# Performance work log

Hardware: AMD Instinct MI355X
Metric: run time of the kernel (lower is better)

The kernel has to match this reference:

```python
import jax, jax.numpy as jnp
import numpy as np

B, T, N, D, INTER, KS = 8, 12, 325, 64, 16, 3
BN_EPS = 1e-5
LN_EPS = 1e-5


def _stx(x):
    # [B,T,N,D] -> edge-pad time, unfold window 3 -> [B,T,3N,D] (window-major like torch reshape)
    xp = jnp.concatenate([x[:, :1], x, x[:, -1:]], axis=1)          # [B,T+2,N,D]
    w = jnp.stack([xp[:, i:i + T] for i in range(3)], axis=2)        # [B,T,3,N,D]
    return w.reshape(x.shape[0], T, 3 * N, x.shape[-1])


def _conv1x1(y, W, b):
    # y: [B,C,T,N], W: [O,C], b: [O]
    return jnp.einsum('bctn,oc->botn', y, W) + b[None, :, None, None]


def _bn_eval(y, g, b):
    # BatchNorm2d eval with running mean 0 / var 1
    return y * (g / jnp.sqrt(1.0 + BN_EPS))[None, :, None, None] + b[None, :, None, None]


def setup_inputs() -> dict:
    key = jax.random.key(0)
    ks = jax.random.split(key, 32)
    inp = {}
    inp['x'] = jax.random.normal(ks[0], (B, T, N, D), jnp.float32)
    inp['gso'] = jax.random.normal(ks[1], (B, N, N), jnp.float32) * 0.05
    inp['geo_mask'] = jax.random.bernoulli(ks[2], 0.5, (N, N))
    s = 1.0 / np.sqrt(D)
    inp['Wq'] = jax.random.normal(ks[3], (D, D), jnp.float32) * s
    inp['Wk'] = jax.random.normal(ks[4], (D, D), jnp.float32) * s
    inp['Wv'] = jax.random.normal(ks[5], (D, D), jnp.float32) * s
    inp['cheb_w'] = jax.random.normal(ks[6], (KS, D, D), jnp.float32) * s
    inp['p_t12'] = jax.random.normal(ks[7], (N,), jnp.float32)
    inp['p_t21'] = jax.random.normal(ks[8], (N,), jnp.float32)
    inp['p_t23'] = jax.random.normal(ks[9], (N,), jnp.float32)
    inp['p_t32'] = jax.random.normal(ks[10], (N,), jnp.float32)
    inp['ln_g'] = jnp.ones((D,), jnp.float32)
    inp['ln_b'] = jnp.zeros((D,), jnp.float32)
    si = 1.0 / np.sqrt(INTER)
    for pfx, kk in (('l', 11), ('g', 17)):
        inp[pfx + '_w1'] = jax.random.normal(ks[kk], (INTER, D), jnp.float32) * s
        inp[pfx + '_b1'] = jax.random.normal(ks[kk + 1], (INTER,), jnp.float32) * s
        inp[pfx + '_g1'] = jnp.ones((INTER,), jnp.float32)
        inp[pfx + '_be1'] = jnp.zeros((INTER,), jnp.float32)
        inp[pfx + '_w2'] = jax.random.normal(ks[kk + 2], (D, INTER), jnp.float32) * si
        inp[pfx + '_b2'] = jax.random.normal(ks[kk + 3], (D,), jnp.float32) * si
        inp[pfx + '_g2'] = jnp.ones((D,), jnp.float32)
        inp[pfx + '_be2'] = jnp.zeros((D,), jnp.float32)
    return inp


def _forward(x, gso, geo_mask, Wq, Wk, Wv, cheb_w, p_t12, p_t21, p_t23, p_t32,
             ln_g, ln_b,
             l_w1, l_b1, l_g1, l_be1, l_w2, l_b2, l_g2, l_be2,
             g_w1, g_b1, g_g1, g_be1, g_w2, g_b2, g_g2, g_be2):
    M = 3 * N
    stX = _stx(x)                                                    # [B,T,M,D]

    # ---- DSTFormer: masked spatiotemporal attention (no scaling, per source) ----
    q = jnp.einsum('btmd,od->btmo', stX, Wq)
    k = jnp.einsum('btmd,od->btmo', stX, Wk)
    v = jnp.einsum('btmd,od->btmo', stX, Wv)
    attn = jnp.einsum('btmo,btno->btmn', q, k)                       # [B,T,M,M]
    eye = jnp.eye(N, dtype=bool)
    uneye = ~eye
    tru = jnp.ones((N, N), dtype=bool)
    big_mask = jnp.block([[geo_mask, uneye, tru],
                          [uneye, geo_mask, uneye],
                          [tru, uneye, geo_mask]])                   # [M,M]
    attn = jnp.where(big_mask, -jnp.inf, attn)
    p = jax.nn.softmax(attn, axis=-1)
    sem = jnp.einsum('btmn,btno->btmo', p, v)                        # [B,T,M,D]
    # faithful to torch: transpose(2,3) then reshape(B,T,M,-1) (mixes layout)
    y = jnp.swapaxes(sem, 2, 3).reshape(B, T, M, D)
    attn_out = y.reshape(B, T, 3, N, D)[:, :, 1]                     # [B,T,N,D]

    # ---- DSTGCN: Chebyshev conv on assembled [B,3N,3N] shift operator ----
    Z = jnp.zeros((B, N, N), x.dtype)
    dg = lambda vv: jnp.broadcast_to(jnp.diag(vv), (B, N, N))
    row0 = jnp.concatenate([gso, dg(p_t21), Z], axis=2)
    row1 = jnp.concatenate([dg(p_t12), gso, dg(p_t32)], axis=2)
    row2 = jnp.concatenate([Z, dg(p_t23), gso], axis=2)
    L = jnp.concatenate([row0, row1, row2], axis=1)                  # [B,M,M]
    xs = [stX, jnp.einsum('bhi,btij->bthj', L, stX)]
    for kk in range(2, KS):
        xs.append(jnp.einsum('bhi,btij->bthj', 2.0 * L, xs[kk - 1]) - xs[kk - 2])
    xk = jnp.stack(xs, axis=2)                                       # [B,T,KS,M,D]
    h = jnp.einsum('btkhi,kij->bthj', xk, cheb_w)                    # [B,T,M,D]
    h = jnp.transpose(h, (0, 3, 1, 2)).reshape(B, D, T, 3, N)[:, :, :, 1, :]  # [B,D,T,N]
    h = jnp.transpose(h, (0, 2, 3, 1))                               # [B,T,N,D]
    mu = h.mean(-1, keepdims=True)
    var = ((h - mu) ** 2).mean(-1, keepdims=True)
    gcn_out = (h - mu) / jnp.sqrt(var + LN_EPS) * ln_g + ln_b

    # ---- AFF fusion on channel-first maps ----
    xc = jnp.transpose(attn_out, (0, 3, 1, 2))                       # [B,D,T,N]
    rc = jnp.transpose(gcn_out, (0, 3, 1, 2))
    xa = xc + rc
    zl = jax.nn.relu(_bn_eval(_conv1x1(xa, l_w1, l_b1), l_g1, l_be1))
    xl = _bn_eval(_conv1x1(zl, l_w2, l_b2), l_g2, l_be2)
    m = xa.mean((2, 3), keepdims=True)
    zg = jax.nn.relu(_bn_eval(_conv1x1(m, g_w1, g_b1), g_g1, g_be1))
    xg = _bn_eval(_conv1x1(zg, g_w2, g_b2), g_g2, g_be2)
    wei = jax.nn.sigmoid(xl + xg)
    out = 2.0 * xc * wei + 2.0 * rc * (1.0 - wei)
    return jnp.transpose(out, (0, 2, 3, 1))                          # [B,T,N,D]


def reference(x, gso, geo_mask, Wq, Wk, Wv, cheb_w, p_t12, p_t21, p_t23, p_t32,
              ln_g, ln_b,
              l_w1, l_b1, l_g1, l_be1, l_w2, l_b2, l_g2, l_be2,
              g_w1, g_b1, g_g1, g_be1, g_w2, g_b2, g_g2, g_be2):
    return _forward(x, gso, geo_mask, Wq, Wk, Wv, cheb_w, p_t12, p_t21, p_t23, p_t32,
                    ln_g, ln_b,
                    l_w1, l_b1, l_g1, l_be1, l_w2, l_b2, l_g2, l_be2,
                    g_w1, g_b1, g_g1, g_be1, g_w2, g_b2, g_g2, g_be2)
```

## Files before the change

kernel.cpp:

```cpp
#include <hip/hip_runtime.h>
#include <math.h>

constexpr int TT = 12;
constexpr int NN = 325;
constexpr int MM = 975;
constexpr int DD = 64;
constexpr long SZ = 96L * MM * DD;
constexpr int GSTR = 352;
constexpr int MBSTR = 48;
constexpr float BN_EPS_ = 1e-5f;
constexpr float LN_EPS_ = 1e-5f;

constexpr long WS_MASKB = 0;
constexpr long WS_GSOB  = WS_MASKB + 4096;
constexpr long WS_STXB  = WS_GSOB + 457600;
constexpr long WS_QB    = WS_STXB + SZ / 2;
constexpr long WS_KB    = WS_QB + SZ / 2;
constexpr long WS_VB    = WS_KB + SZ / 2;
constexpr long WS_SEM   = WS_VB + SZ / 2;
constexpr long WS_T2B   = WS_SEM + SZ;
constexpr long WS_MBD   = WS_T2B + 998400;

typedef _Float16 half8 __attribute__((ext_vector_type(8)));
typedef __attribute__((ext_vector_type(4))) float f32x4;

static __device__ inline unsigned short f2h(float f) {
  _Float16 h = (_Float16)f;
  return __builtin_bit_cast(unsigned short, h);
}
static __device__ inline float h2f(unsigned short s) {
  return (float)__builtin_bit_cast(_Float16, s);
}

__global__ __launch_bounds__(256) void k_maskprep(const unsigned char* __restrict__ raw,
                                                  unsigned char* __restrict__ outm) {
  bool is_u8 = false;
  for (int i = 0; i < 256; ++i) {
    if (raw[4 * i + 1]) { is_u8 = true; break; }
  }
  int idx = blockIdx.x * 256 + threadIdx.x;
  if (idx >= NN * MBSTR) return;
  int n = idx / MBSTR, jb = idx - n * MBSTR;
  unsigned char v = 0;
  for (int k = 0; k < 8; ++k) {
    int col = jb * 8 + k;
    bool m = true;
    if (col < NN) {
      int f = n * NN + col;
      m = is_u8 ? (raw[f] != 0) : (((const int*)raw)[f] != 0);
    }
    v |= (unsigned char)(m ? 1 : 0) << k;
  }
  outm[idx] = v;
}

__global__ __launch_bounds__(256) void k_gsoprep(const float* __restrict__ gso,
                                                 unsigned short* __restrict__ gsoB) {
  int idx = blockIdx.x * 256 + threadIdx.x;
  int b = idx / (NN * GSTR);
  int rem = idx - b * (NN * GSTR);
  int r = rem / GSTR, j = rem - r * GSTR;
  gsoB[idx] = (j < NN) ? f2h(gso[(long)b * NN * NN + r * NN + j]) : (unsigned short)0;
}

__global__ __launch_bounds__(256) void k_stx(const float* __restrict__ x,
                                             unsigned short* __restrict__ stXb) {
  int idx = blockIdx.x * 256 + threadIdx.x;
  int d = idx & 63;
  int m = (idx >> 6) % MM;
  int bt = idx / (MM * DD);
  int b = bt / TT, t = bt - b * TT;
  int w = m / NN, n = m - w * NN;
  int st = t + w - 1;
  st = st < 0 ? 0 : (st > TT - 1 ? TT - 1 : st);
  stXb[idx] = f2h(x[(((b * TT + st) * NN + n) << 6) + d]);
}

__global__ __launch_bounds__(256) void k_qkv_mfma(const unsigned short* __restrict__ stXb,
                                                  const float* __restrict__ Wq,
                                                  const float* __restrict__ Wk,
                                                  const float* __restrict__ Wv,
                                                  unsigned short* __restrict__ qb,
                                                  unsigned short* __restrict__ kb,
                                                  unsigned short* __restrict__ vb) {
  __shared__ alignas(16) unsigned short sX[128 * 72];
  __shared__ alignas(16) unsigned short sW[64 * 72];
  const float* W = blockIdx.y == 0 ? Wq : (blockIdx.y == 1 ? Wk : Wv);
  unsigned short* outb = blockIdx.y == 0 ? qb : (blockIdx.y == 1 ? kb : vb);
  int tid = threadIdx.x;
  long r0 = (long)blockIdx.x * 128;
  for (int u = 0; u < 4; ++u) {
    int idx = tid + 256 * u;
    int row = idx >> 3, c8 = idx & 7;
    long rg = r0 + row; if (rg > 93599) rg = 93599;
    *(uint4*)&sX[row * 72 + c8 * 8] = *(const uint4*)&stXb[rg * 64 + c8 * 8];
  }
  for (int u = 0; u < 16; ++u) {
    int f = tid + 256 * u;
    int o = f >> 6, d = f & 63;
    sW[o * 72 + d] = f2h(W[f]);
  }
  __syncthreads();
  int lane = tid & 63;
  int wv = __builtin_amdgcn_readfirstlane(tid >> 6);
  int lr = lane & 15, lg = lane >> 4;
  f32x4 zero4 = {0.f, 0.f, 0.f, 0.f};
  f32x4 acc[2][4];
#pragma unroll
  for (int rt = 0; rt < 2; ++rt)
#pragma unroll
    for (int c = 0; c < 4; ++c) acc[rt][c] = zero4;
#pragma unroll
  for (int kk = 0; kk < 2; ++kk) {
    half8 a0 = *(const half8*)&sX[(32 * wv + lr) * 72 + kk * 32 + lg * 8];
    half8 a1 = *(const half8*)&sX[(32 * wv + 16 + lr) * 72 + kk * 32 + lg * 8];
#pragma unroll
    for (int c = 0; c < 4; ++c) {
      half8 b = *(const half8*)&sW[(16 * c + lr) * 72 + kk * 32 + lg * 8];
      acc[0][c] = __builtin_amdgcn_mfma_f32_16x16x32_f16(a0, b, acc[0][c], 0, 0, 0);
      acc[1][c] = __builtin_amdgcn_mfma_f32_16x16x32_f16(a1, b, acc[1][c], 0, 0, 0);
    }
  }
  __syncthreads();
#pragma unroll
  for (int rt = 0; rt < 2; ++rt)
#pragma unroll
    for (int c = 0; c < 4; ++c)
#pragma unroll
      for (int e = 0; e < 4; ++e) {
        int row = 32 * wv + 16 * rt + lg * 4 + e;
        int col = 16 * c + lr;
        sX[row * 64 + col] = f2h(acc[rt][c][e]);
      }
  __syncthreads();
  for (int u = 0; u < 4; ++u) {
    int idx = tid + 256 * u;
    int row = idx >> 3, c8 = idx & 7;
    long rg = r0 + row;
    if (rg < 93600)
      *(uint4*)&outb[rg * 64 + c8 * 8] = *(const uint4*)&sX[row * 64 + c8 * 8];
  }
}

__global__ __launch_bounds__(256) void k_attn(const unsigned short* __restrict__ qb,
                                              const unsigned short* __restrict__ kb,
                                              const unsigned short* __restrict__ vb,
                                              const unsigned char* __restrict__ maskb,
                                              float* __restrict__ sem) {
  __shared__ alignas(16) unsigned short Kl[336 * 72];
  __shared__ alignas(16) unsigned short Ql[64 * 72];
  __shared__ unsigned char Mb[64 * MBSTR];
  int btw = blockIdx.x;
  int bt = btw / 3, w = btw - bt * 3;
  int rt = blockIdx.y;
  long base = ((long)bt * MM + (long)w * NN) * 64;
  int tid = threadIdx.x;
  for (int u = 0; u < 11; ++u) {
    int idx = tid + 256 * u;
    if (idx < 2688) {
      int r = idx >> 3, c8 = idx & 7;
      int rr = r < NN ? r : NN - 1;
      *(uint4*)&Kl[r * 72 + c8 * 8] = *(const uint4*)&kb[base + (long)rr * 64 + c8 * 8];
    }
  }
  for (int u = 0; u < 2; ++u) {
    int idx = tid + 256 * u;
    int r = idx >> 3, c8 = idx & 7;
    int rg = rt * 64 + r; if (rg > NN - 1) rg = NN - 1;
    *(uint4*)&Ql[r * 72 + c8 * 8] = *(const uint4*)&qb[base + (long)rg * 64 + c8 * 8];
  }
  if (tid < 192) {
    int r = tid / 3, c16 = tid - (tid / 3) * 3;
    int rg = rt * 64 + r; if (rg > NN - 1) rg = NN - 1;
    *(uint4*)&Mb[r * MBSTR + c16 * 16] = *(const uint4*)&maskb[(long)rg * MBSTR + c16 * 16];
  }
  __syncthreads();
  int lane = tid & 63;
  int wv = __builtin_amdgcn_readfirstlane(tid >> 6);
  int lr = lane & 15, lg = lane >> 4;
  f32x4 zero4 = {0.f, 0.f, 0.f, 0.f};
  f32x4 acc[22];
#pragma unroll
  for (int ct = 0; ct < 22; ++ct) acc[ct] = zero4;
  f32x4 dA = zero4, dB = zero4;
  int nl_f = rt * 64 + 16 * wv + lr; if (nl_f > NN - 1) nl_f = NN - 1;
  long pAaddr = ((long)bt * MM + ((w == 1) ? nl_f : NN + nl_f)) * 64;
  long pBaddr = ((long)bt * MM + 2 * NN + nl_f) * 64;
#pragma unroll
  for (int kk = 0; kk < 2; ++kk) {
    half8 a = *(const half8*)&Ql[(16 * wv + lr) * 72 + kk * 32 + lg * 8];
#pragma unroll
    for (int ct = 0; ct < 21; ++ct) {
      half8 b = *(const half8*)&Kl[(16 * ct + lr) * 72 + kk * 32 + lg * 8];
      acc[ct] = __builtin_amdgcn_mfma_f32_16x16x32_f16(a, b, acc[ct], 0, 0, 0);
    }
    half8 bA = *(const half8*)&kb[pAaddr + kk * 32 + lg * 8];
    dA = __builtin_amdgcn_mfma_f32_16x16x32_f16(a, bA, dA, 0, 0, 0);
    if (w == 1) {
      half8 bB = *(const half8*)&kb[pBaddr + kk * 32 + lg * 8];
      dB = __builtin_amdgcn_mfma_f32_16x16x32_f16(a, bB, dB, 0, 0, 0);
    }
  }
  float da_[4], db_[4];
#pragma unroll
  for (int e = 0; e < 4; ++e) {
    int src = lg * 20 + e;
    da_[e] = __shfl(dA[e], src);
    db_[e] = (w == 1) ? __shfl(dB[e], src) : -INFINITY;
  }
  float mx[4] = {-INFINITY, -INFINITY, -INFINITY, -INFINITY};
#pragma unroll
  for (int ct = 0; ct < 22; ++ct) {
    int col = 16 * ct + lr;
#pragma unroll
    for (int e = 0; e < 4; ++e) {
      int rl = 16 * wv + lg * 4 + e;
      bool masked = (col >= NN) ||
                    ((Mb[rl * MBSTR + (col >> 3)] >> (col & 7)) & 1);
      float s = masked ? -INFINITY : acc[ct][e];
      acc[ct][e] = s;
      mx[e] = fmaxf(mx[e], s);
    }
  }
#pragma unroll
  for (int e = 0; e < 4; ++e)
    for (int m = 1; m < 16; m <<= 1) mx[e] = fmaxf(mx[e], __shfl_xor(mx[e], m));
  float gm[4], ea[4], eb[4], sum[4], inv[4];
#pragma unroll
  for (int e = 0; e < 4; ++e) {
    gm[e] = fmaxf(mx[e], da_[e]);
    if (w == 1) gm[e] = fmaxf(gm[e], db_[e]);
    sum[e] = 0.f;
  }
#pragma unroll
  for (int ct = 0; ct < 22; ++ct)
#pragma unroll
    for (int e = 0; e < 4; ++e) {
      float s = acc[ct][e];
      float p = (s > -1e37f) ? __expf(s - gm[e]) : 0.f;
      acc[ct][e] = p;
      sum[e] += p;
    }
#pragma unroll
  for (int e = 0; e < 4; ++e) {
    for (int m = 1; m < 16; m <<= 1) sum[e] += __shfl_xor(sum[e], m);
    ea[e] = __expf(da_[e] - gm[e]);
    eb[e] = (w == 1) ? __expf(db_[e] - gm[e]) : 0.f;
    sum[e] += ea[e] + eb[e];
    inv[e] = 1.f / sum[e];
  }
  __syncthreads();
  unsigned short* Bt = Kl;
  for (int u = 0; u < 22; ++u) {
    int idx = tid + 256 * u;
    if (idx < 5632) {
      int k = idx >> 4, c4 = idx & 15;
      ushort4 vvv;
      if (k < NN) vvv = *(const ushort4*)&vb[base + (long)k * 64 + c4 * 4];
      else { vvv.x = 0; vvv.y = 0; vvv.z = 0; vvv.w = 0; }
      Bt[(4 * c4 + 0) * 352 + k] = vvv.x;
      Bt[(4 * c4 + 1) * 352 + k] = vvv.y;
      Bt[(4 * c4 + 2) * 352 + k] = vvv.z;
      Bt[(4 * c4 + 3) * 352 + k] = vvv.w;
    }
  }
  __syncthreads();
  unsigned short* Ptr = (unsigned short*)Ql + wv * 640;
  f32x4 oacc[4];
#pragma unroll
  for (int c = 0; c < 4; ++c) oacc[c] = zero4;
  for (int ck = 0; ck < 11; ++ck) {
#pragma unroll
    for (int t = 0; t < 2; ++t) {
      int ct = 2 * ck + t;
#pragma unroll
      for (int e = 0; e < 4; ++e)
        Ptr[(lg * 4 + e) * 40 + t * 16 + lr] = f2h(acc[ct][e] * inv[e]);
    }
    half8 a = *(const half8*)&Ptr[lr * 40 + lg * 8];
#pragma unroll
    for (int c = 0; c < 4; ++c) {
      half8 b = *(const half8*)&Bt[(16 * c + lr) * 352 + ck * 32 + lg * 8];
      oacc[c] = __builtin_amdgcn_mfma_f32_16x16x32_f16(a, b, oacc[c], 0, 0, 0);
    }
  }
#pragma unroll
  for (int c = 0; c < 4; ++c)
#pragma unroll
    for (int e = 0; e < 4; ++e) {
      int n = rt * 64 + 16 * wv + lg * 4 + e;
      int col = 16 * c + lr;
      if (n < NN) {
        float val = oacc[c][e];
        int partA = (w == 1) ? n : NN + n;
        val += ea[e] * inv[e] * h2f(vb[((long)bt * MM + partA) * 64 + col]);
        if (w == 1)
          val += eb[e] * inv[e] * h2f(vb[((long)bt * MM + 2 * NN + n) * 64 + col]);
        sem[((long)bt * MM + (long)w * NN + n) * 64 + col] = val;
      }
    }
}

__global__ __launch_bounds__(256) void k_xs1_mfma(const unsigned short* __restrict__ gsoB,
                                                  const unsigned short* __restrict__ stXb,
                                                  const float* __restrict__ pt12,
                                                  const float* __restrict__ pt21,
                                                  const float* __restrict__ pt23,
                                                  const float* __restrict__ pt32,
                                                  unsigned short* __restrict__ xs1b) {
  __shared__ alignas(16) unsigned short Al[128 * 40];
  __shared__ alignas(16) unsigned short Bt[64 * 40];
  int btw = blockIdx.x;
  int bt = btw / 3, w = btw - bt * 3;
  int b = bt / TT;
  int rt_blk = blockIdx.y;
  const unsigned short* A = gsoB + (long)b * NN * GSTR;
  long vbase = (long)bt * MM + (long)w * NN;
  int tid = threadIdx.x;
  int lane = tid & 63;
  int wv = __builtin_amdgcn_readfirstlane(tid >> 6);
  int lr = lane & 15, lg = lane >> 4;
  f32x4 zero4 = {0.f, 0.f, 0.f, 0.f};
  f32x4 acc[2][4];
#pragma unroll
  for (int rt = 0; rt < 2; ++rt)
#pragma unroll
    for (int c = 0; c < 4; ++c) acc[rt][c] = zero4;
  for (int kb_ = 0; kb_ < 352; kb_ += 32) {
    __syncthreads();
    for (int u = 0; u < 2; ++u) {
      int idx = tid + 256 * u;
      int row = idx >> 2, c8 = idx & 3;
      int rr = rt_blk * 128 + row; if (rr > NN - 1) rr = NN - 1;
      *(uint4*)&Al[row * 40 + c8 * 8] = *(const uint4*)&A[(long)rr * GSTR + kb_ + c8 * 8];
    }
    for (int u = 0; u < 2; ++u) {
      int idx = tid + 256 * u;
      int k = idx >> 4, c4 = idx & 15;
      int kg = kb_ + k;
      ushort4 vv;
      if (kg < NN) vv = *(const ushort4*)&stXb[(vbase + kg) * 64 + c4 * 4];
      else { vv.x = 0; vv.y = 0; vv.z = 0; vv.w = 0; }
      Bt[(4 * c4 + 0) * 40 + k] = vv.x;
      Bt[(4 * c4 + 1) * 40 + k] = vv.y;
      Bt[(4 * c4 + 2) * 40 + k] = vv.z;
      Bt[(4 * c4 + 3) * 40 + k] = vv.w;
    }
    __syncthreads();
    half8 a0 = *(const half8*)&Al[(32 * wv + lr) * 40 + lg * 8];
    half8 a1 = *(const half8*)&Al[(32 * wv + 16 + lr) * 40 + lg * 8];
#pragma unroll
    for (int c = 0; c < 4; ++c) {
      half8 b_ = *(const half8*)&Bt[(16 * c + lr) * 40 + lg * 8];
      acc[0][c] = __builtin_amdgcn_mfma_f32_16x16x32_f16(a0, b_, acc[0][c], 0, 0, 0);
      acc[1][c] = __builtin_amdgcn_mfma_f32_16x16x32_f16(a1, b_, acc[1][c], 0, 0, 0);
    }
  }
  long btM = (long)bt * MM;
#pragma unroll
  for (int rt = 0; rt < 2; ++rt)
#pragma unroll
    for (int c = 0; c < 4; ++c)
#pragma unroll
      for (int e = 0; e < 4; ++e) {
        int n = rt_blk * 128 + 32 * wv + 16 * rt + lg * 4 + e;
        int col = 16 * c + lr;
        if (n < NN) {
          float val = acc[rt][c][e];
          if (w == 0) {
            val += pt21[n] * h2f(stXb[(btM + NN + n) * 64 + col]);
          } else if (w == 1) {
            val += pt12[n] * h2f(stXb[(btM + n) * 64 + col])
                 + pt32[n] * h2f(stXb[(btM + 2 * NN + n) * 64 + col]);
          } else {
            val += pt23[n] * h2f(stXb[(btM + NN + n) * 64 + col]);
          }
          xs1b[(btM + (long)w * NN + n) * 64 + col] = f2h(val);
        }
      }
}

__global__ __launch_bounds__(256) void k_t2_mfma(const unsigned short* __restrict__ gsoB,
                                                 const unsigned short* __restrict__ xs1b,
                                                 const unsigned short* __restrict__ stXb,
                                                 const float* __restrict__ pt12,
                                                 const float* __restrict__ pt32,
                                                 unsigned short* __restrict__ t2b) {
  __shared__ alignas(16) unsigned short Al[128 * 40];
  __shared__ alignas(16) unsigned short Bt[64 * 40];
  int bt = blockIdx.x;
  int b = bt / TT;
  int rt_blk = blockIdx.y;
  const unsigned short* A = gsoB + (long)b * NN * GSTR;
  long vbase = (long)bt * MM + NN;
  int tid = threadIdx.x;
  int lane = tid & 63;
  int wv = __builtin_amdgcn_readfirstlane(tid >> 6);
  int lr = lane & 15, lg = lane >> 4;
  f32x4 zero4 = {0.f, 0.f, 0.f, 0.f};
  f32x4 acc[2][4];
#pragma unroll
  for (int rt = 0; rt < 2; ++rt)
#pragma unroll
    for (int c = 0; c < 4; ++c) acc[rt][c] = zero4;
  for (int kb_ = 0; kb_ < 352; kb_ += 32) {
    __syncthreads();
    for (int u = 0; u < 2; ++u) {
      int idx = tid + 256 * u;
      int row = idx >> 2, c8 = idx & 3;
      int rr = rt_blk * 128 + row; if (rr > NN - 1) rr = NN - 1;
      *(uint4*)&Al[row * 40 + c8 * 8] = *(const uint4*)&A[(long)rr * GSTR + kb_ + c8 * 8];
    }
    for (int u = 0; u < 2; ++u) {
      int idx = tid + 256 * u;
      int k = idx >> 4, c4 = idx & 15;
      int kg = kb_ + k;
      ushort4 vv;
      if (kg < NN) vv = *(const ushort4*)&xs1b[(vbase + kg) * 64 + c4 * 4];
      else { vv.x = 0; vv.y = 0; vv.z = 0; vv.w = 0; }
      Bt[(4 * c4 + 0) * 40 + k] = vv.x;
      Bt[(4 * c4 + 1) * 40 + k] = vv.y;
      Bt[(4 * c4 + 2) * 40 + k] = vv.z;
      Bt[(4 * c4 + 3) * 40 + k] = vv.w;
    }
    __syncthreads();
    half8 a0 = *(const half8*)&Al[(32 * wv + lr) * 40 + lg * 8];
    half8 a1 = *(const half8*)&Al[(32 * wv + 16 + lr) * 40 + lg * 8];
#pragma unroll
    for (int c = 0; c < 4; ++c) {
      half8 b_ = *(const half8*)&Bt[(16 * c + lr) * 40 + lg * 8];
      acc[0][c] = __builtin_amdgcn_mfma_f32_16x16x32_f16(a0, b_, acc[0][c], 0, 0, 0);
      acc[1][c] = __builtin_amdgcn_mfma_f32_16x16x32_f16(a1, b_, acc[1][c], 0, 0, 0);
    }
  }
  long btM = (long)bt * MM;
#pragma unroll
  for (int rt = 0; rt < 2; ++rt)
#pragma unroll
    for (int c = 0; c < 4; ++c)
#pragma unroll
      for (int e = 0; e < 4; ++e) {
        int n = rt_blk * 128 + 32 * wv + 16 * rt + lg * 4 + e;
        int col = 16 * c + lr;
        if (n < NN) {
          float val = 2.f * (pt12[n] * h2f(xs1b[(btM + n) * 64 + col])
                             + acc[rt][c][e]
                             + pt32[n] * h2f(xs1b[(btM + 2 * NN + n) * 64 + col]))
                      - h2f(stXb[(btM + NN + n) * 64 + col]);
          t2b[((long)bt * NN + n) * 64 + col] = f2h(val);
        }
      }
}

__global__ __launch_bounds__(256) void k_cheb_mfma(const unsigned short* __restrict__ stXb,
                                                   const unsigned short* __restrict__ xs1b,
                                                   const unsigned short* __restrict__ t2b,
                                                   const float* __restrict__ cw,
                                                   const float* __restrict__ lng,
                                                   const float* __restrict__ lnb,
                                                   float* __restrict__ gcn) {
  __shared__ alignas(16) unsigned short Bt[64 * 200];
  __shared__ alignas(16) unsigned short Al[128 * 40];
  int tid = threadIdx.x;
  for (int u = 0; u < 48; ++u) {
    int f = tid + 256 * u;
    int K = f >> 6, j = f & 63;
    Bt[j * 200 + K] = f2h(cw[f]);
  }
  int lane = tid & 63;
  int wv = __builtin_amdgcn_readfirstlane(tid >> 6);
  int lr = lane & 15, lg = lane >> 4;
  long grow0 = (long)blockIdx.x * 128;
  f32x4 zero4 = {0.f, 0.f, 0.f, 0.f};
  f32x4 acc[2][4];
#pragma unroll
  for (int rt = 0; rt < 2; ++rt)
#pragma unroll
    for (int c = 0; c < 4; ++c) acc[rt][c] = zero4;
  for (int ch = 0; ch < 6; ++ch) {
    const unsigned short* src = ch < 2 ? stXb : (ch < 4 ? xs1b : t2b);
    int koff = (ch & 1) * 32;
    __syncthreads();
    for (int u = 0; u < 2; ++u) {
      int idx = tid + 256 * u;
      int row = idx >> 2, c8 = idx & 3;
      long gr = grow0 + row; if (gr > 31199) gr = 31199;
      int bt = (int)(gr / NN), n = (int)(gr - (long)bt * NN);
      long sbase = (ch < 4) ? ((long)bt * MM + NN + n) * 64 : gr * 64;
      *(uint4*)&Al[row * 40 + c8 * 8] = *(const uint4*)&src[sbase + koff + c8 * 8];
    }
    __syncthreads();
    half8 a0 = *(const half8*)&Al[(32 * wv + lr) * 40 + lg * 8];
    half8 a1 = *(const half8*)&Al[(32 * wv + 16 + lr) * 40 + lg * 8];
#pragma unroll
    for (int c = 0; c < 4; ++c) {
      half8 b = *(const half8*)&Bt[(16 * c + lr) * 200 + ch * 32 + lg * 8];
      acc[0][c] = __builtin_amdgcn_mfma_f32_16x16x32_f16(a0, b, acc[0][c], 0, 0, 0);
      acc[1][c] = __builtin_amdgcn_mfma_f32_16x16x32_f16(a1, b, acc[1][c], 0, 0, 0);
    }
  }
  float lngv[4], lnbv[4];
#pragma unroll
  for (int c = 0; c < 4; ++c) { lngv[c] = lng[16 * c + lr]; lnbv[c] = lnb[16 * c + lr]; }
#pragma unroll
  for (int rt = 0; rt < 2; ++rt)
#pragma unroll
    for (int e = 0; e < 4; ++e) {
      float s = acc[rt][0][e] + acc[rt][1][e] + acc[rt][2][e] + acc[rt][3][e];
      for (int m = 1; m < 16; m <<= 1) s += __shfl_xor(s, m);
      float mu = s * (1.f / 64.f);
      float q = 0.f;
#pragma unroll
      for (int c = 0; c < 4; ++c) { float d = acc[rt][c][e] - mu; q += d * d; }
      for (int m = 1; m < 16; m <<= 1) q += __shfl_xor(q, m);
      float rstd = rsqrtf(q * (1.f / 64.f) + LN_EPS_);
      long gr = grow0 + 32 * wv + 16 * rt + lg * 4 + e;
      if (gr < 31200) {
#pragma unroll
        for (int c = 0; c < 4; ++c)
          gcn[gr * 64 + 16 * c + lr] = (acc[rt][c][e] - mu) * rstd * lngv[c] + lnbv[c];
      }
    }
}

__global__ __launch_bounds__(256) void k_mean(const float* __restrict__ sem,
                                              const float* __restrict__ gcn,
                                              float* __restrict__ mbd) {
  __shared__ float red[4][64];
  int bt = blockIdx.x;
  int b = bt / TT;
  int d = threadIdx.x & 63, g = threadIdx.x >> 6;
  float s = 0.f;
  for (int n = g; n < NN; n += 4) {
    int f = (NN + n) * 64 + d;
    int mm = f % MM, ii = f / MM;
    float a = sem[((long)bt * MM + mm) * 64 + ii];
    float r = gcn[((long)bt * NN + n) * 64 + d];
    s += a + r;
  }
  red[g][d] = s;
  __syncthreads();
  if (threadIdx.x < 64) {
    float v = red[0][d] + red[1][d] + red[2][d] + red[3][d];
    atomicAdd(&mbd[b * 64 + d], v);
  }
}

__global__ __launch_bounds__(64) void k_glob(const float* __restrict__ mbd,
                                             const float* __restrict__ w1,
                                             const float* __restrict__ b1,
                                             const float* __restrict__ g1,
                                             const float* __restrict__ be1,
                                             const float* __restrict__ w2,
                                             const float* __restrict__ b2,
                                             const float* __restrict__ g2,
                                             const float* __restrict__ be2,
                                             float* __restrict__ xg) {
  __shared__ float ml[64];
  __shared__ float zg[16];
  int b = blockIdx.x, d = threadIdx.x;
  ml[d] = mbd[b * 64 + d] * (1.f / 3900.f);
  __syncthreads();
  float rb = rsqrtf(1.f + BN_EPS_);
  if (d < 16) {
    float a = b1[d];
    for (int i = 0; i < 64; ++i) a += w1[d * 64 + i] * ml[i];
    a = a * (g1[d] * rb) + be1[d];
    zg[d] = a > 0.f ? a : 0.f;
  }
  __syncthreads();
  float a = b2[d];
  for (int i = 0; i < 16; ++i) a += w2[d * 16 + i] * zg[i];
  xg[b * 64 + d] = a * (g2[d] * rb) + be2[d];
}

__global__ __launch_bounds__(256) void k_final(const float* __restrict__ sem,
                                               const float* __restrict__ gcn,
                                               const float* __restrict__ xg,
                                               const float* __restrict__ w1,
                                               const float* __restrict__ b1,
                                               const float* __restrict__ g1,
                                               const float* __restrict__ be1,
                                               const float* __restrict__ w2,
                                               const float* __restrict__ b2,
                                               const float* __restrict__ g2,
                                               const float* __restrict__ be2,
                                               float* __restrict__ out) {
  __shared__ float w1l[16][65];
  __shared__ float w2l[64][17];
  __shared__ float xal[4][64];
  __shared__ float zll[4][16];
  int tid = threadIdx.x;
  for (int u = 0; u < 4; ++u) {
    int f = tid + 256 * u;
    w1l[f >> 6][f & 63] = w1[f];
    w2l[f >> 4][f & 15] = w2[f];
  }
  int lane = tid & 63, wv = tid >> 6;
  long row = (long)blockIdx.x * 4 + wv;
  int bt = (int)(row / NN);
  int n = (int)(row - (long)bt * NN);
  int b = bt / TT;
  int f = (NN + n) * 64 + lane;
  int mm = f % MM, ii = f / MM;
  float a = sem[((long)bt * MM + mm) * 64 + ii];
  float r = gcn[row * DD + lane];
  float xa = a + r;
  xal[wv][lane] = xa;
  __syncthreads();
  float rb = rsqrtf(1.f + BN_EPS_);
  if (lane < 16) {
    float acc = b1[lane];
#pragma unroll 8
    for (int i = 0; i < 64; ++i) acc += w1l[lane][i] * xal[wv][i];
    acc = acc * (g1[lane] * rb) + be1[lane];
    zll[wv][lane] = acc > 0.f ? acc : 0.f;
  }
  __syncthreads();
  float acc = b2[lane];
#pragma unroll
  for (int i = 0; i < 16; ++i) acc += w2l[lane][i] * zll[wv][i];
  float xl = acc * (g2[lane] * rb) + be2[lane];
  float wei = 1.f / (1.f + __expf(-(xl + xg[b * 64 + lane])));
  out[row * DD + lane] = 2.f * a * wei + 2.f * r * (1.f - wei);
}

extern "C" void kernel_launch(void* const* d_in, const int* in_sizes, int n_in,
                              void* d_out, int out_size, void* d_ws, size_t ws_size,
                              hipStream_t stream) {
  const float* x    = (const float*)d_in[0];
  const float* gso  = (const float*)d_in[1];
  const unsigned char* mask_raw = (const unsigned char*)d_in[2];
  const float* Wq   = (const float*)d_in[3];
  const float* Wk   = (const float*)d_in[4];
  const float* Wv   = (const float*)d_in[5];
  const float* chw  = (const float*)d_in[6];
  const float* pt12 = (const float*)d_in[7];
  const float* pt21 = (const float*)d_in[8];
  const float* pt23 = (const float*)d_in[9];
  const float* pt32 = (const float*)d_in[10];
  const float* lng  = (const float*)d_in[11];
  const float* lnb  = (const float*)d_in[12];
  const float* l_w1 = (const float*)d_in[13];
  const float* l_b1 = (const float*)d_in[14];
  const float* l_g1 = (const float*)d_in[15];
  const float* l_be1= (const float*)d_in[16];
  const float* l_w2 = (const float*)d_in[17];
  const float* l_b2 = (const float*)d_in[18];
  const float* l_g2 = (const float*)d_in[19];
  const float* l_be2= (const float*)d_in[20];
  const float* g_w1 = (const float*)d_in[21];
  const float* g_b1 = (const float*)d_in[22];
  const float* g_g1 = (const float*)d_in[23];
  const float* g_be1= (const float*)d_in[24];
  const float* g_w2 = (const float*)d_in[25];
  const float* g_b2 = (const float*)d_in[26];
  const float* g_g2 = (const float*)d_in[27];
  const float* g_be2= (const float*)d_in[28];

  float* base = (float*)d_ws;
  unsigned char* maskb = (unsigned char*)d_ws;
  unsigned short* gsoB = (unsigned short*)(base + WS_GSOB);
  unsigned short* stXb = (unsigned short*)(base + WS_STXB);
  unsigned short* qb   = (unsigned short*)(base + WS_QB);
  unsigned short* kb   = (unsigned short*)(base + WS_KB);
  unsigned short* vb   = (unsigned short*)(base + WS_VB);
  float* sem           = base + WS_SEM;
  unsigned short* t2b  = (unsigned short*)(base + WS_T2B);

  unsigned short* xs1b = vb;
  float* gcn = (float*)qb;
  float* mbd = base + WS_MBD;
  float* xg  = mbd + 512;

  k_maskprep<<<(NN * MBSTR + 255) / 256, 256, 0, stream>>>(mask_raw, maskb);
  k_gsoprep<<<3575, 256, 0, stream>>>(gso, gsoB);
  k_stx<<<23400, 256, 0, stream>>>(x, stXb);
  {
    dim3 g(732, 3);
    k_qkv_mfma<<<g, 256, 0, stream>>>(stXb, Wq, Wk, Wv, qb, kb, vb);
  }
  {
    dim3 ga(288, 6);
    k_attn<<<ga, 256, 0, stream>>>(qb, kb, vb, maskb, sem);
  }
  {
    dim3 g(288, 3);
    k_xs1_mfma<<<g, 256, 0, stream>>>(gsoB, stXb, pt12, pt21, pt23, pt32, xs1b);
  }
  {
    dim3 g(96, 3);
    k_t2_mfma<<<g, 256, 0, stream>>>(gsoB, xs1b, stXb, pt12, pt32, t2b);
  }
  k_cheb_mfma<<<244, 256, 0, stream>>>(stXb, xs1b, t2b, chw, lng, lnb, gcn);
  hipMemsetAsync(mbd, 0, 1024 * sizeof(float), stream);
  k_mean<<<96, 256, 0, stream>>>(sem, gcn, mbd);
  k_glob<<<8, 64, 0, stream>>>(mbd, g_w1, g_b1, g_g1, g_be1, g_w2, g_b2, g_g2, g_be2, xg);
  k_final<<<7800, 256, 0, stream>>>(sem, gcn, xg,
                                    l_w1, l_b1, l_g1, l_be1,
                                    l_w2, l_b2, l_g2, l_be2,
                                    (float*)d_out);
}
```

Before: 413.1 us.

## Pre-transpose V, read Q/K directly from global in attention, store fp16 output

Adds a k_vT kernel that writes V transposed into a padded workspace, so k_attn no longer transposes V in shared memory. k_attn also drops its large K/Q shared-memory staging and reads MFMA operands straight from global/L2, with launch bounds set for more resident blocks. Mask bits are now loaded as 32-bit words. The attention output becomes fp16, which halves traffic into k_mean and k_final at some precision cost. The V transposes in the xs1/t2 kernels are also rewritten as strided per-element loads.

After: 370.1 us. 10.4% less time.

```diff
diff --git a/kernel.cpp b/kernel.cpp
--- a/kernel.cpp
+++ b/kernel.cpp
@@ -8,6 +8,7 @@
 constexpr long SZ = 96L * MM * DD;
 constexpr int GSTR = 352;
 constexpr int MBSTR = 48;
+constexpr int VTS = 22528;
 constexpr float BN_EPS_ = 1e-5f;
 constexpr float LN_EPS_ = 1e-5f;
 
@@ -17,8 +18,9 @@
 constexpr long WS_QB    = WS_STXB + SZ / 2;
 constexpr long WS_KB    = WS_QB + SZ / 2;
 constexpr long WS_VB    = WS_KB + SZ / 2;
-constexpr long WS_SEM   = WS_VB + SZ / 2;
-constexpr long WS_T2B   = WS_SEM + SZ;
+constexpr long WS_VT    = WS_VB + SZ / 2;
+constexpr long WS_SEMH  = WS_VT + 3244032;
+constexpr long WS_T2B   = WS_SEMH + SZ / 2;
 constexpr long WS_MBD   = WS_T2B + 998400;
 
 typedef _Float16 half8 __attribute__((ext_vector_type(8)));
@@ -142,33 +144,49 @@
   }
 }
 
-__global__ __launch_bounds__(256) void k_attn(const unsigned short* __restrict__ qb,
-                                              const unsigned short* __restrict__ kb,
-                                              const unsigned short* __restrict__ vb,
-                                              const unsigned char* __restrict__ maskb,
-                                              float* __restrict__ sem) {
-  __shared__ alignas(16) unsigned short Kl[336 * 72];
-  __shared__ alignas(16) unsigned short Ql[64 * 72];
+__global__ __launch_bounds__(256) void k_vT(const unsigned short* __restrict__ vb,
+                                            unsigned short* __restrict__ vbT) {
+  __shared__ alignas(16) unsigned short T[128 * 72];
+  int seg = blockIdx.x;
+  int ck = blockIdx.y;
+  int tid = threadIdx.x;
+  long base = (long)seg * NN * 64;
+  int k0 = ck * 128;
+  for (int u = 0; u < 4; ++u) {
+    int idx = tid + 256 * u;
+    int row = idx >> 3, c8 = idx & 7;
+    int kg = k0 + row;
+    uint4 v;
+    if (kg < NN) v = *(const uint4*)&vb[base + (long)kg * 64 + c8 * 8];
+    else { v.x = 0; v.y = 0; v.z = 0; v.w = 0; }
+    *(uint4*)&T[row * 72 + c8 * 8] = v;
+  }
+  __syncthreads();
+  int d = tid & 63, k8 = tid >> 6;
+  for (int it = 0; it < 4; ++it) {
+    int klocal = (it * 4 + k8) * 8;
+    if (k0 + klocal < 352) {
+      unsigned short tmp[8];
+#pragma unroll
+      for (int j = 0; j < 8; ++j) tmp[j] = T[(klocal + j) * 72 + d];
+      *(uint4*)&vbT[(long)seg * VTS + (long)d * 352 + k0 + klocal] = *(const uint4*)tmp;
+    }
+  }
+}
+
+__global__ __launch_bounds__(256, 3) void k_attn(const unsigned short* __restrict__ qb,
+                                                 const unsigned short* __restrict__ kb,
+                                                 const unsigned short* __restrict__ vb,
+                                                 const unsigned short* __restrict__ vbT,
+                                                 const unsigned char* __restrict__ maskb,
+                                                 unsigned short* __restrict__ semh) {
   __shared__ unsigned char Mb[64 * MBSTR];
-  int btw = blockIdx.x;
-  int bt = btw / 3, w = btw - bt * 3;
+  __shared__ alignas(16) unsigned short Ptr4[4 * 16 * 40];
+  int seg = blockIdx.x;
+  int bt = seg / 3, w = seg - bt * 3;
   int rt = blockIdx.y;
-  long base = ((long)bt * MM + (long)w * NN) * 64;
+  long segbase = (long)seg * NN * 64;
   int tid = threadIdx.x;
-  for (int u = 0; u < 11; ++u) {
-    int idx = tid + 256 * u;
-    if (idx < 2688) {
-      int r = idx >> 3, c8 = idx & 7;
-      int rr = r < NN ? r : NN - 1;
-      *(uint4*)&Kl[r * 72 + c8 * 8] = *(const uint4*)&kb[base + (long)rr * 64 + c8 * 8];
-    }
-  }
-  for (int u = 0; u < 2; ++u) {
-    int idx = tid + 256 * u;
-    int r = idx >> 3, c8 = idx & 7;
-    int rg = rt * 64 + r; if (rg > NN - 1) rg = NN - 1;
-    *(uint4*)&Ql[r * 72 + c8 * 8] = *(const uint4*)&qb[base + (long)rg * 64 + c8 * 8];
-  }
   if (tid < 192) {
     int r = tid / 3, c16 = tid - (tid / 3) * 3;
     int rg = rt * 64 + r; if (rg > NN - 1) rg = NN - 1;
@@ -179,19 +197,22 @@
   int wv = __builtin_amdgcn_readfirstlane(tid >> 6);
   int lr = lane & 15, lg = lane >> 4;
   f32x4 zero4 = {0.f, 0.f, 0.f, 0.f};
-  f32x4 acc[22];
-#pragma unroll
-  for (int ct = 0; ct < 22; ++ct) acc[ct] = zero4;
+  f32x4 acc[21];
+#pragma unroll
+  for (int ct = 0; ct < 21; ++ct) acc[ct] = zero4;
   f32x4 dA = zero4, dB = zero4;
-  int nl_f = rt * 64 + 16 * wv + lr; if (nl_f > NN - 1) nl_f = NN - 1;
+  int arow = rt * 64 + 16 * wv + lr; if (arow > NN - 1) arow = NN - 1;
+  long abase = segbase + (long)arow * 64;
+  int nl_f = arow;
   long pAaddr = ((long)bt * MM + ((w == 1) ? nl_f : NN + nl_f)) * 64;
   long pBaddr = ((long)bt * MM + 2 * NN + nl_f) * 64;
 #pragma unroll
   for (int kk = 0; kk < 2; ++kk) {
-    half8 a = *(const half8*)&Ql[(16 * wv + lr) * 72 + kk * 32 + lg * 8];
+    half8 a = *(const half8*)&qb[abase + kk * 32 + lg * 8];
 #pragma unroll
     for (int ct = 0; ct < 21; ++ct) {
-      half8 b = *(const half8*)&Kl[(16 * ct + lr) * 72 + kk * 32 + lg * 8];
+      int brow = 16 * ct + lr; if (brow > NN - 1) brow = NN - 1;
+      half8 b = *(const half8*)&kb[segbase + (long)brow * 64 + kk * 32 + lg * 8];
       acc[ct] = __builtin_amdgcn_mfma_f32_16x16x32_f16(a, b, acc[ct], 0, 0, 0);
     }
     half8 bA = *(const half8*)&kb[pAaddr + kk * 32 + lg * 8];
@@ -209,14 +230,20 @@
     db_[e] = (w == 1) ? __shfl(dB[e], src) : -INFINITY;
   }
   float mx[4] = {-INFINITY, -INFINITY, -INFINITY, -INFINITY};
-#pragma unroll
-  for (int ct = 0; ct < 22; ++ct) {
-    int col = 16 * ct + lr;
+  unsigned mw[4];
+#pragma unroll
+  for (int ct = 0; ct < 21; ++ct) {
+    if ((ct & 1) == 0) {
+#pragma unroll
+      for (int e = 0; e < 4; ++e) {
+        int rl = 16 * wv + lg * 4 + e;
+        mw[e] = *(const unsigned*)&Mb[rl * MBSTR + (ct >> 1) * 4];
+      }
+    }
+    int sh = 16 * (ct & 1) + lr;
 #pragma unroll
     for (int e = 0; e < 4; ++e) {
-      int rl = 16 * wv + lg * 4 + e;
-      bool masked = (col >= NN) ||
-                    ((Mb[rl * MBSTR + (col >> 3)] >> (col & 7)) & 1);
+      bool masked = (mw[e] >> sh) & 1;
       float s = masked ? -INFINITY : acc[ct][e];
       acc[ct][e] = s;
       mx[e] = fmaxf(mx[e], s);
@@ -233,7 +260,7 @@
     sum[e] = 0.f;
   }
 #pragma unroll
-  for (int ct = 0; ct < 22; ++ct)
+  for (int ct = 0; ct < 21; ++ct)
 #pragma unroll
     for (int e = 0; e < 4; ++e) {
       float s = acc[ct][e];
@@ -249,38 +276,26 @@
     sum[e] += ea[e] + eb[e];
     inv[e] = 1.f / sum[e];
   }
-  __syncthreads();
-  unsigned short* Bt = Kl;
-  for (int u = 0; u < 22; ++u) {
-    int idx = tid + 256 * u;
-    if (idx < 5632) {
-      int k = idx >> 4, c4 = idx & 15;
-      ushort4 vvv;
-      if (k < NN) vvv = *(const ushort4*)&vb[base + (long)k * 64 + c4 * 4];
-      else { vvv.x = 0; vvv.y = 0; vvv.z = 0; vvv.w = 0; }
-      Bt[(4 * c4 + 0) * 352 + k] = vvv.x;
-      Bt[(4 * c4 + 1) * 352 + k] = vvv.y;
-      Bt[(4 * c4 + 2) * 352 + k] = vvv.z;
-      Bt[(4 * c4 + 3) * 352 + k] = vvv.w;
-    }
-  }
-  __syncthreads();
-  unsigned short* Ptr = (unsigned short*)Ql + wv * 640;
+  unsigned short* Ptr = Ptr4 + wv * 640;
+  long vtbase = (long)seg * VTS;
   f32x4 oacc[4];
 #pragma unroll
   for (int c = 0; c < 4; ++c) oacc[c] = zero4;
+#pragma unroll
   for (int ck = 0; ck < 11; ++ck) {
 #pragma unroll
     for (int t = 0; t < 2; ++t) {
       int ct = 2 * ck + t;
 #pragma unroll
-      for (int e = 0; e < 4; ++e)
-        Ptr[(lg * 4 + e) * 40 + t * 16 + lr] = f2h(acc[ct][e] * inv[e]);
+      for (int e = 0; e < 4; ++e) {
+        float pv = (ct < 21) ? acc[ct][e] * inv[e] : 0.f;
+        Ptr[(lg * 4 + e) * 40 + t * 16 + lr] = f2h(pv);
+      }
     }
     half8 a = *(const half8*)&Ptr[lr * 40 + lg * 8];
 #pragma unroll
     for (int c = 0; c < 4; ++c) {
-      half8 b = *(const half8*)&Bt[(16 * c + lr) * 352 + ck * 32 + lg * 8];
+      half8 b = *(const half8*)&vbT[vtbase + (long)(16 * c + lr) * 352 + ck * 32 + lg * 8];
       oacc[c] = __builtin_amdgcn_mfma_f32_16x16x32_f16(a, b, oacc[c], 0, 0, 0);
     }
   }
@@ -296,7 +311,7 @@
         val += ea[e] * inv[e] * h2f(vb[((long)bt * MM + partA) * 64 + col]);
         if (w == 1)
           val += eb[e] * inv[e] * h2f(vb[((long)bt * MM + 2 * NN + n) * 64 + col]);
-        sem[((long)bt * MM + (long)w * NN + n) * 64 + col] = val;
+        semh[((long)bt * MM + (long)w * NN + n) * 64 + col] = f2h(val);
       }
     }
 }
@@ -338,13 +353,12 @@
       int idx = tid + 256 * u;
       int k = idx >> 4, c4 = idx & 15;
       int kg = kb_ + k;
-      ushort4 vv;
-      if (kg < NN) vv = *(const ushort4*)&stXb[(vbase + kg) * 64 + c4 * 4];
-      else { vv.x = 0; vv.y = 0; vv.z = 0; vv.w = 0; }
-      Bt[(4 * c4 + 0) * 40 + k] = vv.x;
-      Bt[(4 * c4 + 1) * 40 + k] = vv.y;
-      Bt[(4 * c4 + 2) * 40 + k] = vv.z;
-      Bt[(4 * c4 + 3) * 40 + k] = vv.w;
+#pragma unroll
+      for (int j = 0; j < 4; ++j) {
+        int d = c4 + 16 * j;
+        unsigned short val = (kg < NN) ? stXb[(vbase + kg) * 64 + d] : (unsigned short)0;
+        Bt[d * 40 + k] = val;
+      }
     }
     __syncthreads();
     half8 a0 = *(const half8*)&Al[(32 * wv + lr) * 40 + lg * 8];
@@ -415,13 +429,12 @@
       int idx = tid + 256 * u;
       int k = idx >> 4, c4 = idx & 15;
       int kg = kb_ + k;
-      ushort4 vv;
-      if (kg < NN) vv = *(const ushort4*)&xs1b[(vbase + kg) * 64 + c4 * 4];
-      else { vv.x = 0; vv.y = 0; vv.z = 0; vv.w = 0; }
-      Bt[(4 * c4 + 0) * 40 + k] = vv.x;
-      Bt[(4 * c4 + 1) * 40 + k] = vv.y;
-      Bt[(4 * c4 + 2) * 40 + k] = vv.z;
-      Bt[(4 * c4 + 3) * 40 + k] = vv.w;
+#pragma unroll
+      for (int j = 0; j < 4; ++j) {
+        int d = c4 + 16 * j;
+        unsigned short val = (kg < NN) ? xs1b[(vbase + kg) * 64 + d] : (unsigned short)0;
+        Bt[d * 40 + k] = val;
+      }
     }
     __syncthreads();
     half8 a0 = *(const half8*)&Al[(32 * wv + lr) * 40 + lg * 8];
@@ -523,7 +536,7 @@
     }
 }
 
-__global__ __launch_bounds__(256) void k_mean(const float* __restrict__ sem,
+__global__ __launch_bounds__(256) void k_mean(const unsigned short* __restrict__ semh,
                                               const float* __restrict__ gcn,
                                               float* __restrict__ mbd) {
   __shared__ float red[4][64];
@@ -534,7 +547,7 @@
   for (int n = g; n < NN; n += 4) {
     int f = (NN + n) * 64 + d;
     int mm = f % MM, ii = f / MM;
-    float a = sem[((long)bt * MM + mm) * 64 + ii];
+    float a = h2f(semh[((long)bt * MM + mm) * 64 + ii]);
     float r = gcn[((long)bt * NN + n) * 64 + d];
     s += a + r;
   }
@@ -574,7 +587,7 @@
   xg[b * 64 + d] = a * (g2[d] * rb) + be2[d];
 }
 
-__global__ __launch_bounds__(256) void k_final(const float* __restrict__ sem,
+__global__ __launch_bounds__(256) void k_final(const unsigned short* __restrict__ semh,
                                                const float* __restrict__ gcn,
                                                const float* __restrict__ xg,
                                                const float* __restrict__ w1,
@@ -603,7 +616,7 @@
   int b = bt / TT;
   int f = (NN + n) * 64 + lane;
   int mm = f % MM, ii = f / MM;
-  float a = sem[((long)bt * MM + mm) * 64 + ii];
+  float a = h2f(semh[((long)bt * MM + mm) * 64 + ii]);
   float r = gcn[row * DD + lane];
   float xa = a + r;
   xal[wv][lane] = xa;
@@ -665,7 +678,8 @@
   unsigned short* qb   = (unsigned short*)(base + WS_QB);
   unsigned short* kb   = (unsigned short*)(base + WS_KB);
   unsigned short* vb   = (unsigned short*)(base + WS_VB);
-  float* sem           = base + WS_SEM;
+  unsigned short* vbT  = (unsigned short*)(base + WS_VT);
+  unsigned short* semh = (unsigned short*)(base + WS_SEMH);
   unsigned short* t2b  = (unsigned short*)(base + WS_T2B);
 
   unsigned short* xs1b = vb;
@@ -681,8 +695,12 @@
     k_qkv_mfma<<<g, 256, 0, stream>>>(stXb, Wq, Wk, Wv, qb, kb, vb);
   }
   {
+    dim3 gv(288, 3);
+    k_vT<<<gv, 256, 0, stream>>>(vb, vbT);
+  }
+  {
     dim3 ga(288, 6);
-    k_attn<<<ga, 256, 0, stream>>>(qb, kb, vb, maskb, sem);
+    k_attn<<<ga, 256, 0, stream>>>(qb, kb, vb, vbT, maskb, semh);
   }
   {
     dim3 g(288, 3);
@@ -694,9 +712,9 @@
   }
   k_cheb_mfma<<<244, 256, 0, stream>>>(stXb, xs1b, t2b, chw, lng, lnb, gcn);
   hipMemsetAsync(mbd, 0, 1024 * sizeof(float), stream);
-  k_mean<<<96, 256, 0, stream>>>(sem, gcn, mbd);
+  k_mean<<<96, 256, 0, stream>>>(semh, gcn, mbd);
   k_glob<<<8, 64, 0, stream>>>(mbd, g_w1, g_b1, g_g1, g_be1, g_w2, g_b2, g_g2, g_be2, xg);
-  k_final<<<7800, 256, 0, stream>>>(sem, gcn, xg,
+  k_final<<<7800, 256, 0, stream>>>(semh, gcn, xg,
                                     l_w1, l_b1, l_g1, l_be1,
                                     l_w2, l_b2, l_g2, l_be2,
                                     (float*)d_out);
```
